# Kernel optimization log

Hardware: AMD Instinct MI355X
Metric: run time of the kernel (lower is better)

## Reference

```python
import jax, jax.numpy as jnp
import numpy as np

DN = ('NCHW', 'OIHW', 'NCHW')

def _conv(x, w, b=None):
    # x: [P, C, H, W], w: [1, C, k, k] -> [P, 1, H, W] with SAME padding
    y = jax.lax.conv_general_dilated(x, w, (1, 1), 'SAME', dimension_numbers=DN)
    if b is not None:
        y = y + b[None, :, None, None]
    return y

def setup_inputs() -> dict:
    key = jax.random.key(0)
    ks = jax.random.split(key, 6)
    T, P, H, W = 36, 64, 128, 256
    K = 5
    inputs = jax.random.normal(ks[0], (T, P, H, W), dtype=jnp.float32)
    w_reset = 0.1 * jax.random.normal(ks[1], (1, 2, K, K), dtype=jnp.float32)
    b_reset = jnp.zeros((1,), dtype=jnp.float32)
    w_update = 0.1 * jax.random.normal(ks[2], (1, 2, K, K), dtype=jnp.float32)
    b_update = jnp.zeros((1,), dtype=jnp.float32)
    w_out = 0.1 * jax.random.normal(ks[3], (1, 2, K, K), dtype=jnp.float32)
    gam = jnp.ones((P,), dtype=jnp.float32)
    add_weights = 0.02 * jax.random.normal(ks[4], (P, H, W), dtype=jnp.float32)
    bias = jnp.zeros((H, W), dtype=jnp.float32)
    return {"inputs": inputs, "w_reset": w_reset, "b_reset": b_reset,
            "w_update": w_update, "b_update": b_update, "w_out": w_out,
            "gam": gam, "add_weights": add_weights, "bias": bias}

def reference(inputs, w_reset, b_reset, w_update, b_update, w_out, gam, add_weights, bias):
    # inputs: [T, P, H, W]; renormalize by per-plant scale gam
    x = gam[None, :, None, None] * inputs
    x = x[:, :, None]  # [T, P, 1, H, W] (channel dim = 1)
    h0 = jnp.zeros_like(x[0])  # [P, 1, H, W]

    def step(h, xt):
        stacked = jnp.concatenate([xt, h], axis=1)  # [P, 2, H, W]
        u = jax.nn.sigmoid(_conv(stacked, w_update, b_update))  # update gate
        r = jax.nn.sigmoid(_conv(stacked, w_reset, b_reset))    # reset gate
        c = _conv(jnp.concatenate([xt, r * h], axis=1), w_out)  # candidate (no bias, no act)
        h_new = h * (1.0 - u) + c * u
        return h_new, h_new

    _, states = jax.lax.scan(step, h0, x)  # [T, P, 1, H, W]
    s = states[:, :, 0]  # [T, P, H, W]
    # final layer (additive=False, rnn_act=None): tanh then per-plant spatial weights
    xs = jnp.tanh(s) * add_weights[None]
    out_y = xs.sum(axis=1) + bias[None]  # [T, H, W]
    return out_y, xs
```

## Files before the change

kernel.cpp:

```cpp
#include <hip/hip_runtime.h>

constexpr int T = 36, P = 64, H = 128, W = 256;
constexpr int HW  = H * W;
constexpr int PHW = P * HW;

constexpr int TH   = 16;
constexpr int NB   = 8;
constexpr int NBLK = P * NB;
constexpr int SR = 24, SC = 268;
constexpr int RR = 20;

constexpr long long TMO_ARRIVE = 3000000;
constexpr long long TMO_STEP   = 1000000;

typedef float vfloat4 __attribute__((ext_vector_type(4)));

__device__ __forceinline__ float fast_sigmoid(float z) {
    float e = __expf(-z);
    return __builtin_amdgcn_rcpf(1.0f + e);
}
__device__ __forceinline__ float fast_tanh(float x) {
    float e = __expf(-2.0f * fabsf(x));
    float t = (1.0f - e) * __builtin_amdgcn_rcpf(1.0f + e);
    return copysignf(t, x);
}

__device__ __forceinline__ void lds_store4(float* d, float4 v) {
    *(float2*)d       = make_float2(v.x, v.y);
    *(float2*)(d + 2) = make_float2(v.z, v.w);
}

__global__ __launch_bounds__(512, 4) void gru_all(
    const float* __restrict__ inputs, const float* __restrict__ gam,
    const float* __restrict__ w_update, const float* __restrict__ b_update,
    const float* __restrict__ w_reset,  const float* __restrict__ b_reset,
    const float* __restrict__ w_out,    const float* __restrict__ add_w,
    float* __restrict__ xs, float* __restrict__ hhalo, int* __restrict__ flags)
{
    __shared__ __align__(16) float sx[SR][SC];
    __shared__ __align__(16) float sh[SR][SC];
    __shared__ __align__(16) float srh[RR][SC];
    __shared__ int s_nowait;

    const int tid  = threadIdx.x;
    const int bid  = blockIdx.x;
    const int p    = bid >> 3;
    const int band = bid & 7;
    const int y0   = band * TH;

    const float gamma = gam[p];
    const float bu = b_update[0];
    const float br = b_reset[0];

    const int cg = tid & 63, rbb = tid >> 6;
    const int ox = 4 * cg,   oy  = 2 * rbb;

    if (tid == 0) {
        s_nowait = 0;
        __hip_atomic_fetch_add(&flags[NBLK], 1, __ATOMIC_RELAXED, __HIP_MEMORY_SCOPE_AGENT);
        const long long t0 = (long long)__builtin_amdgcn_s_memrealtime();
        while (__hip_atomic_load(&flags[NBLK], __ATOMIC_RELAXED, __HIP_MEMORY_SCOPE_AGENT) < NBLK) {
            __builtin_amdgcn_s_sleep(16);
            if ((long long)__builtin_amdgcn_s_memrealtime() - t0 > TMO_ARRIVE) { s_nowait = 1; break; }
        }
    }

    float4 aw4[2];
    #pragma unroll
    for (int k = 0; k < 2; ++k)
        aw4[k] = *(const float4*)&add_w[(size_t)p * HW + (y0 + oy + k) * W + ox];

    for (int s = tid; s < SR * SC; s += 512) {
        (&sx[0][0])[s] = 0.f;
        (&sh[0][0])[s] = 0.f;
    }
    __syncthreads();
    {
        const float* xt = inputs + (size_t)p * HW;
        for (int s = tid; s < SR * 64; s += 512) {
            const int r = s >> 6, c4 = s & 63;
            const int gy = y0 + r - 4;
            if ((unsigned)gy < (unsigned)H) {
                float4 v = *(const float4*)&xt[gy * W + 4 * c4];
                v.x *= gamma; v.y *= gamma; v.z *= gamma; v.w *= gamma;
                lds_store4(&sx[r][6 + 4 * c4], v);
            }
        }
    }
    __syncthreads();

    #pragma unroll 1
    for (int t = 0; t < T; ++t) {
        if (tid < 330) {
            const int b5 = tid / 66;
            const int g  = tid - b5 * 66;
            const int r0 = 4 * b5;
            const int c0 = 4 * g;
            float racc[4][4], hold[4][4];
            #pragma unroll
            for (int k = 0; k < 4; ++k)
                #pragma unroll
                for (int c = 0; c < 4; ++c) racc[k][c] = br;
            #pragma unroll
            for (int ir = 0; ir < 8; ++ir) {
                const float4 xa = *(const float4*)&sx[r0 + ir][c0];
                const float4 xb = *(const float4*)&sx[r0 + ir][c0 + 4];
                const float4 ha = *(const float4*)&sh[r0 + ir][c0];
                const float4 hb = *(const float4*)&sh[r0 + ir][c0 + 4];
                const float vx[8] = {xa.x, xa.y, xa.z, xa.w, xb.x, xb.y, xb.z, xb.w};
                const float vh[8] = {ha.x, ha.y, ha.z, ha.w, hb.x, hb.y, hb.z, hb.w};
                if (ir >= 2 && ir <= 5) {
                    #pragma unroll
                    for (int c = 0; c < 4; ++c) hold[ir - 2][c] = vh[c + 2];
                }
                #pragma unroll
                for (int k = 0; k < 4; ++k) {
                    const int dy = ir - k;
                    if (dy >= 0 && dy <= 4) {
                        #pragma unroll
                        for (int dx = 0; dx < 5; ++dx) {
                            const float wx = w_reset[dy * 5 + dx];
                            const float wh = w_reset[25 + dy * 5 + dx];
                            #pragma unroll
                            for (int c = 0; c < 4; ++c) {
                                racc[k][c] = fmaf(vx[c + dx], wx, racc[k][c]);
                                racc[k][c] = fmaf(vh[c + dx], wh, racc[k][c]);
                            }
                        }
                    }
                }
            }
            #pragma unroll
            for (int k = 0; k < 4; ++k) {
                float4 v;
                v.x = fast_sigmoid(racc[k][0]) * hold[k][0];
                v.y = fast_sigmoid(racc[k][1]) * hold[k][1];
                v.z = fast_sigmoid(racc[k][2]) * hold[k][2];
                v.w = fast_sigmoid(racc[k][3]) * hold[k][3];
                lds_store4(&srh[r0 + k][c0 + 2], v);
            }
        }
        __syncthreads();

        float4 hn4[2];
        {
            float uacc[2][4], cacc[2][4], hold[2][4];
            #pragma unroll
            for (int k = 0; k < 2; ++k)
                #pragma unroll
                for (int c = 0; c < 4; ++c) { uacc[k][c] = bu; cacc[k][c] = 0.f; }
            #pragma unroll
            for (int ir = 0; ir < 6; ++ir) {
                const int sr = oy + 2 + ir;
                const float4 xa = *(const float4*)&sx[sr][ox + 4];
                const float4 xb = *(const float4*)&sx[sr][ox + 8];
                const float4 ha = *(const float4*)&sh[sr][ox + 4];
                const float4 hb = *(const float4*)&sh[sr][ox + 8];
                const float4 ra = *(const float4*)&srh[oy + ir][ox + 4];
                const float4 rb = *(const float4*)&srh[oy + ir][ox + 8];
                const float vx[8] = {xa.x, xa.y, xa.z, xa.w, xb.x, xb.y, xb.z, xb.w};
                const float vh[8] = {ha.x, ha.y, ha.z, ha.w, hb.x, hb.y, hb.z, hb.w};
                const float vr[8] = {ra.x, ra.y, ra.z, ra.w, rb.x, rb.y, rb.z, rb.w};
                if (ir == 2) {
                    #pragma unroll
                    for (int c = 0; c < 4; ++c) hold[0][c] = vh[c + 2];
                }
                if (ir == 3) {
                    #pragma unroll
                    for (int c = 0; c < 4; ++c) hold[1][c] = vh[c + 2];
                }
                #pragma unroll
                for (int k = 0; k < 2; ++k) {
                    const int dy = ir - k;
                    if (dy >= 0 && dy <= 4) {
                        #pragma unroll
                        for (int dx = 0; dx < 5; ++dx) {
                            const float wux = w_update[dy * 5 + dx];
                            const float wuh = w_update[25 + dy * 5 + dx];
                            const float wox = w_out[dy * 5 + dx];
                            const float wor = w_out[25 + dy * 5 + dx];
                            #pragma unroll
                            for (int c = 0; c < 4; ++c) {
                                uacc[k][c] = fmaf(vx[c + dx], wux, uacc[k][c]);
                                uacc[k][c] = fmaf(vh[c + dx], wuh, uacc[k][c]);
                                cacc[k][c] = fmaf(vx[c + dx], wox, cacc[k][c]);
                                cacc[k][c] = fmaf(vr[c + dx], wor, cacc[k][c]);
                            }
                        }
                    }
                }
            }
            #pragma unroll
            for (int k = 0; k < 2; ++k) {
                float hn[4];
                #pragma unroll
                for (int c = 0; c < 4; ++c) {
                    const float u = fast_sigmoid(uacc[k][c]);
                    hn[c] = hold[k][c] + (cacc[k][c] - hold[k][c]) * u;
                }
                hn4[k] = make_float4(hn[0], hn[1], hn[2], hn[3]);
            }
        }
        __syncthreads();

        #pragma unroll
        for (int k = 0; k < 2; ++k)
            lds_store4(&sh[4 + oy + k][6 + ox], hn4[k]);

        if (rbb < 2 || rbb >= 6) {
            float* hb = hhalo + (size_t)(t & 1) * (NBLK * 2048) + (size_t)bid * 2048;
            #pragma unroll
            for (int k = 0; k < 2; ++k) {
                const int r    = oy + k;
                const int slot = (r < 4) ? r : r - 8;
                float* d = &hb[slot * 256 + ox];
                __hip_atomic_store(&d[0], hn4[k].x, __ATOMIC_RELAXED, __HIP_MEMORY_SCOPE_AGENT);
                __hip_atomic_store(&d[1], hn4[k].y, __ATOMIC_RELAXED, __HIP_MEMORY_SCOPE_AGENT);
                __hip_atomic_store(&d[2], hn4[k].z, __ATOMIC_RELAXED, __HIP_MEMORY_SCOPE_AGENT);
                __hip_atomic_store(&d[3], hn4[k].w, __ATOMIC_RELAXED, __HIP_MEMORY_SCOPE_AGENT);
            }
        }
        {
            float* xso = xs + (size_t)t * PHW + (size_t)p * HW;
            #pragma unroll
            for (int k = 0; k < 2; ++k) {
                vfloat4 v;
                v.x = fast_tanh(hn4[k].x) * aw4[k].x;
                v.y = fast_tanh(hn4[k].y) * aw4[k].y;
                v.z = fast_tanh(hn4[k].z) * aw4[k].z;
                v.w = fast_tanh(hn4[k].w) * aw4[k].w;
                __builtin_nontemporal_store(v, (vfloat4*)&xso[(y0 + oy + k) * W + ox]);
            }
        }
        if (t + 1 < T) {
            const float* xt = inputs + (size_t)(t + 1) * PHW + (size_t)p * HW;
            for (int s = tid; s < SR * 64; s += 512) {
                const int r = s >> 6, c4 = s & 63;
                const int gy = y0 + r - 4;
                if ((unsigned)gy < (unsigned)H) {
                    float4 v = *(const float4*)&xt[gy * W + 4 * c4];
                    v.x *= gamma; v.y *= gamma; v.z *= gamma; v.w *= gamma;
                    lds_store4(&sx[r][6 + 4 * c4], v);
                }
            }
        }

        if (t + 1 >= T) break;

        __syncthreads();

        if (tid == 0)
            __hip_atomic_store(&flags[bid], t + 1, __ATOMIC_RELAXED, __HIP_MEMORY_SCOPE_AGENT);
        if (tid == 0 || tid == 64) {
            const int dir = (tid == 0) ? -1 : 1;
            const int nbd = band + dir;
            if (nbd >= 0 && nbd < NB && !s_nowait) {
                const int nbid = bid + dir;
                const long long t0 = (long long)__builtin_amdgcn_s_memrealtime();
                while (__hip_atomic_load(&flags[nbid], __ATOMIC_RELAXED, __HIP_MEMORY_SCOPE_AGENT) < t + 1) {
                    __builtin_amdgcn_s_sleep(1);
                    if ((long long)__builtin_amdgcn_s_memrealtime() - t0 > TMO_STEP) { s_nowait = 1; break; }
                }
            }
        }
        __syncthreads();

        {
            float* hb0 = hhalo + (size_t)(t & 1) * (NBLK * 2048);
            const int r = tid >> 6, c4 = tid & 63;
            if (r < 4) {
                if (band > 0) {
                    float* src = &hb0[(size_t)(bid - 1) * 2048 + (4 + r) * 256 + 4 * c4];
                    float4 v;
                    v.x = __hip_atomic_load(&src[0], __ATOMIC_RELAXED, __HIP_MEMORY_SCOPE_AGENT);
                    v.y = __hip_atomic_load(&src[1], __ATOMIC_RELAXED, __HIP_MEMORY_SCOPE_AGENT);
                    v.z = __hip_atomic_load(&src[2], __ATOMIC_RELAXED, __HIP_MEMORY_SCOPE_AGENT);
                    v.w = __hip_atomic_load(&src[3], __ATOMIC_RELAXED, __HIP_MEMORY_SCOPE_AGENT);
                    lds_store4(&sh[r][6 + 4 * c4], v);
                }
            } else {
                if (band < 7) {
                    float* src = &hb0[(size_t)(bid + 1) * 2048 + (r - 4) * 256 + 4 * c4];
                    float4 v;
                    v.x = __hip_atomic_load(&src[0], __ATOMIC_RELAXED, __HIP_MEMORY_SCOPE_AGENT);
                    v.y = __hip_atomic_load(&src[1], __ATOMIC_RELAXED, __HIP_MEMORY_SCOPE_AGENT);
                    v.z = __hip_atomic_load(&src[2], __ATOMIC_RELAXED, __HIP_MEMORY_SCOPE_AGENT);
                    v.w = __hip_atomic_load(&src[3], __ATOMIC_RELAXED, __HIP_MEMORY_SCOPE_AGENT);
                    lds_store4(&sh[16 + r][6 + 4 * c4], v);
                }
            }
        }
        __syncthreads();
    }
}

__global__ __launch_bounds__(256) void reduce_out(
    const float* __restrict__ xs, const float* __restrict__ bias,
    float* __restrict__ out_y)
{
    const int i4  = blockIdx.x * 256 + threadIdx.x;
    const int t   = i4 / (HW / 4);
    const int yx4 = i4 - t * (HW / 4);
    const float4* __restrict__ src = (const float4*)(xs + (size_t)t * PHW) + yx4;
    const float4  b4 = ((const float4*)bias)[yx4];
    float a0[4] = {b4.x, b4.y, b4.z, b4.w};
    float a1[4] = {0.f, 0.f, 0.f, 0.f};
    #pragma unroll 8
    for (int p = 0; p < P; p += 2) {
        const float4 v0 = src[(size_t)p * (HW / 4)];
        const float4 v1 = src[(size_t)(p + 1) * (HW / 4)];
        a0[0] += v0.x; a0[1] += v0.y; a0[2] += v0.z; a0[3] += v0.w;
        a1[0] += v1.x; a1[1] += v1.y; a1[2] += v1.z; a1[3] += v1.w;
    }
    ((float4*)out_y)[i4] = make_float4(a0[0] + a1[0], a0[1] + a1[1],
                                       a0[2] + a1[2], a0[3] + a1[3]);
}

extern "C" void kernel_launch(void* const* d_in, const int* in_sizes, int n_in,
                              void* d_out, int out_size, void* d_ws, size_t ws_size,
                              hipStream_t stream) {
    const float* inputs   = (const float*)d_in[0];
    const float* w_reset  = (const float*)d_in[1];
    const float* b_reset  = (const float*)d_in[2];
    const float* w_update = (const float*)d_in[3];
    const float* b_update = (const float*)d_in[4];
    const float* w_out    = (const float*)d_in[5];
    const float* gam      = (const float*)d_in[6];
    const float* add_w    = (const float*)d_in[7];
    const float* bias     = (const float*)d_in[8];

    float* out_y = (float*)d_out;
    float* xs    = out_y + (size_t)T * HW;

    float* hhalo = (float*)d_ws;
    int*   flags = (int*)((char*)d_ws + (size_t)2 * NBLK * 2048 * sizeof(float));

    (void)hipMemsetAsync(flags, 0, (NBLK + 1) * sizeof(int), stream);

    gru_all<<<dim3(NBLK), dim3(512), 0, stream>>>(
        inputs, gam, w_update, b_update, w_reset, b_reset, w_out, add_w,
        xs, hhalo, flags);

    const int nout4 = T * HW / 4;
    reduce_out<<<nout4 / 256, 256, 0, stream>>>(xs, bias, out_y);
}
```

Before: 845.0 us.

## Prefetch next-step inputs into registers and publish step flag earlier

```diff
diff --git a/kernel.cpp b/kernel.cpp
--- a/kernel.cpp
+++ b/kernel.cpp
@@ -7,7 +7,7 @@
 constexpr int TH   = 16;
 constexpr int NB   = 8;
 constexpr int NBLK = P * NB;
-constexpr int SR = 24, SC = 268;
+constexpr int SR = 25, SC = 268;
 constexpr int RR = 20;
 
 constexpr long long TMO_ARRIVE = 3000000;
@@ -77,7 +77,9 @@
     __syncthreads();
     {
         const float* xt = inputs + (size_t)p * HW;
-        for (int s = tid; s < SR * 64; s += 512) {
+        #pragma unroll
+        for (int k = 0; k < 3; ++k) {
+            const int s = tid + 512 * k;
             const int r = s >> 6, c4 = s & 63;
             const int gy = y0 + r - 4;
             if ((unsigned)gy < (unsigned)H) {
@@ -91,30 +93,45 @@
 
     #pragma unroll 1
     for (int t = 0; t < T; ++t) {
-        if (tid < 330) {
-            const int b5 = tid / 66;
-            const int g  = tid - b5 * 66;
-            const int r0 = 4 * b5;
+        float4 xp[3];
+        {
+            const int tc = (t + 1 < T) ? t + 1 : t;
+            const float* xtn = inputs + (size_t)tc * PHW + (size_t)p * HW;
+            #pragma unroll
+            for (int k = 0; k < 3; ++k) {
+                const int s = tid + 512 * k;
+                const int r = s >> 6, c4 = s & 63;
+                const int gy = y0 + r - 4;
+                xp[k] = make_float4(0.f, 0.f, 0.f, 0.f);
+                if ((unsigned)gy < (unsigned)H)
+                    xp[k] = *(const float4*)&xtn[gy * W + 4 * c4];
+            }
+        }
+
+        if (tid < 462) {
+            const int b  = tid / 66;
+            const int g  = tid - 66 * b;
+            const int r0 = 3 * b;
             const int c0 = 4 * g;
-            float racc[4][4], hold[4][4];
-            #pragma unroll
-            for (int k = 0; k < 4; ++k)
+            float racc[3][4], hold[3][4];
+            #pragma unroll
+            for (int k = 0; k < 3; ++k)
                 #pragma unroll
                 for (int c = 0; c < 4; ++c) racc[k][c] = br;
             #pragma unroll
-            for (int ir = 0; ir < 8; ++ir) {
+            for (int ir = 0; ir < 7; ++ir) {
                 const float4 xa = *(const float4*)&sx[r0 + ir][c0];
                 const float4 xb = *(const float4*)&sx[r0 + ir][c0 + 4];
                 const float4 ha = *(const float4*)&sh[r0 + ir][c0];
                 const float4 hb = *(const float4*)&sh[r0 + ir][c0 + 4];
                 const float vx[8] = {xa.x, xa.y, xa.z, xa.w, xb.x, xb.y, xb.z, xb.w};
                 const float vh[8] = {ha.x, ha.y, ha.z, ha.w, hb.x, hb.y, hb.z, hb.w};
-                if (ir >= 2 && ir <= 5) {
+                if (ir >= 2 && ir <= 4) {
                     #pragma unroll
                     for (int c = 0; c < 4; ++c) hold[ir - 2][c] = vh[c + 2];
                 }
                 #pragma unroll
-                for (int k = 0; k < 4; ++k) {
+                for (int k = 0; k < 3; ++k) {
                     const int dy = ir - k;
                     if (dy >= 0 && dy <= 4) {
                         #pragma unroll
@@ -131,13 +148,15 @@
                 }
             }
             #pragma unroll
-            for (int k = 0; k < 4; ++k) {
-                float4 v;
-                v.x = fast_sigmoid(racc[k][0]) * hold[k][0];
-                v.y = fast_sigmoid(racc[k][1]) * hold[k][1];
-                v.z = fast_sigmoid(racc[k][2]) * hold[k][2];
-                v.w = fast_sigmoid(racc[k][3]) * hold[k][3];
-                lds_store4(&srh[r0 + k][c0 + 2], v);
+            for (int k = 0; k < 3; ++k) {
+                if (r0 + k < RR) {
+                    float4 v;
+                    v.x = fast_sigmoid(racc[k][0]) * hold[k][0];
+                    v.y = fast_sigmoid(racc[k][1]) * hold[k][1];
+                    v.z = fast_sigmoid(racc[k][2]) * hold[k][2];
+                    v.w = fast_sigmoid(racc[k][3]) * hold[k][3];
+                    lds_store4(&srh[r0 + k][c0 + 2], v);
+                }
             }
         }
         __syncthreads();
@@ -203,11 +222,7 @@
         }
         __syncthreads();
 
-        #pragma unroll
-        for (int k = 0; k < 2; ++k)
-            lds_store4(&sh[4 + oy + k][6 + ox], hn4[k]);
-
-        if (rbb < 2 || rbb >= 6) {
+        if (t + 1 < T && (rbb < 2 || rbb >= 6)) {
             float* hb = hhalo + (size_t)(t & 1) * (NBLK * 2048) + (size_t)bid * 2048;
             #pragma unroll
             for (int k = 0; k < 2; ++k) {
@@ -220,6 +235,26 @@
                 __hip_atomic_store(&d[3], hn4[k].w, __ATOMIC_RELAXED, __HIP_MEMORY_SCOPE_AGENT);
             }
         }
+        #pragma unroll
+        for (int k = 0; k < 2; ++k)
+            lds_store4(&sh[4 + oy + k][6 + ox], hn4[k]);
+        if (t + 1 < T) {
+            #pragma unroll
+            for (int k = 0; k < 3; ++k) {
+                const int s = tid + 512 * k;
+                const int r = s >> 6, c4 = s & 63;
+                const int gy = y0 + r - 4;
+                if ((unsigned)gy < (unsigned)H) {
+                    float4 v = xp[k];
+                    v.x *= gamma; v.y *= gamma; v.z *= gamma; v.w *= gamma;
+                    lds_store4(&sx[r][6 + 4 * c4], v);
+                }
+            }
+        }
+        __syncthreads();
+
+        if (t + 1 < T && tid == 0)
+            __hip_atomic_store(&flags[bid], t + 1, __ATOMIC_RELAXED, __HIP_MEMORY_SCOPE_AGENT);
         {
             float* xso = xs + (size_t)t * PHW + (size_t)p * HW;
             #pragma unroll
@@ -232,25 +267,8 @@
                 __builtin_nontemporal_store(v, (vfloat4*)&xso[(y0 + oy + k) * W + ox]);
             }
         }
-        if (t + 1 < T) {
-            const float* xt = inputs + (size_t)(t + 1) * PHW + (size_t)p * HW;
-            for (int s = tid; s < SR * 64; s += 512) {
-                const int r = s >> 6, c4 = s & 63;
-                const int gy = y0 + r - 4;
-                if ((unsigned)gy < (unsigned)H) {
-                    float4 v = *(const float4*)&xt[gy * W + 4 * c4];
-                    v.x *= gamma; v.y *= gamma; v.z *= gamma; v.w *= gamma;
-                    lds_store4(&sx[r][6 + 4 * c4], v);
-                }
-            }
-        }
-
         if (t + 1 >= T) break;
 
-        __syncthreads();
-
-        if (tid == 0)
-            __hip_atomic_store(&flags[bid], t + 1, __ATOMIC_RELAXED, __HIP_MEMORY_SCOPE_AGENT);
         if (tid == 0 || tid == 64) {
             const int dir = (tid == 0) ? -1 : 1;
             const int nbd = band + dir;
```

New measurement: 897.2 us. 6.2% more time.
